# Kernel optimization log

Measured on AMD Instinct MI355X. Metric: run time of the kernel, lower is better.

Reference implementation:

```python
import jax, jax.numpy as jnp
import numpy as np

H, W = 80, 80
LOWPASS = 0.3   # 3DGS low-pass filter added to 2D covariance diagonal
NEAR = 0.2      # near-plane cull depth


def quat_to_rot(q):
    # q: [N,4] (w,x,y,z) -> [N,3,3]
    w, x, y, z = q[..., 0], q[..., 1], q[..., 2], q[..., 3]
    return jnp.stack([
        jnp.stack([1 - 2 * (y * y + z * z), 2 * (x * y - w * z), 2 * (x * z + w * y)], -1),
        jnp.stack([2 * (x * y + w * z), 1 - 2 * (x * x + z * z), 2 * (y * z - w * x)], -1),
        jnp.stack([2 * (x * z - w * y), 2 * (y * z + w * x), 1 - 2 * (x * x + y * y)], -1),
    ], -2)


def setup_inputs() -> dict:
    key = jax.random.key(0)
    k1, k2 = jax.random.split(key)
    vsize = 1.25
    def mids(lo, hi, lim):
        g = np.arange(lo, hi + 1e-6, vsize)
        return ((g[:-1] + g[1:]) / 2.0)[:lim]
    xy = mids(-20.0, 20.0, 200)   # 32 midpoints
    zz = mids(-4.0, 4.0, 16)      # 6 midpoints
    X, Y, Z = np.meshgrid(xy, xy, zz, indexing='ij')
    pc_xyz = jnp.asarray(np.stack([X, Y, Z], -1).reshape(-1, 3), jnp.float32)  # [6144,3]
    N = pc_xyz.shape[0]
    B, NC, C = 1, 6, 32
    vox_features = jax.random.normal(k1, (B, N, C), jnp.float32)
    density = jax.random.normal(k2, (B, N), jnp.float32)
    scales = jnp.full((N, 1), float(np.log(vsize)), jnp.float32)
    rots = jnp.concatenate([jnp.ones((N, 1)), jnp.zeros((N, 3))], -1).astype(jnp.float32)
    # 6 surround cameras at origin, yaw = k*60deg; cam axes: x=right, y=up-ish, z=forward
    yaws = np.arange(NC) * (2 * np.pi / NC)
    f = np.stack([np.cos(yaws), np.sin(yaws), np.zeros(NC)], -1)
    r = np.stack([np.sin(yaws), -np.cos(yaws), np.zeros(NC)], -1)
    u = np.cross(f, r)
    Rw2c = np.stack([r, u, f], 1)  # rows are camera axes -> world2cam rotation [NC,3,3]
    cam_rot = jnp.asarray(Rw2c[None], jnp.float32)          # [B,NC,3,3]
    cam_trans = jnp.zeros((B, NC, 3), jnp.float32)          # [B,NC,3]
    cam_intr = jnp.asarray(np.tile(np.array([45.0, 45.0, W / 2.0, H / 2.0], np.float32), (B, NC, 1)))
    return dict(vox_features=vox_features, density=density, cam_rot=cam_rot,
                cam_trans=cam_trans, cam_intr=cam_intr, pc_xyz=pc_xyz,
                scales=scales, rots=rots)


def _render_one(Rcw, t, intr, pc_xyz, Mcov, opacity, feats):
    # Rcw [3,3], t [3], intr [4]; Mcov [N,3,3] = R*diag(s); opacity [N]; feats [N,C]
    fx, fy, cx, cy = intr[0], intr[1], intr[2], intr[3]
    cam = pc_xyz @ Rcw.T + t                    # [N,3] camera-frame means
    tz = jnp.maximum(cam[:, 2], 1e-6)
    valid = (cam[:, 2] > NEAR).astype(pc_xyz.dtype)
    u = fx * cam[:, 0] / tz + cx
    v = fy * cam[:, 1] / tz + cy
    z0 = jnp.zeros_like(tz)
    J = jnp.stack([jnp.stack([fx / tz, z0, -fx * cam[:, 0] / tz ** 2], -1),
                   jnp.stack([z0, fy / tz, -fy * cam[:, 1] / tz ** 2], -1)], -2)  # [N,2,3]
    A = jnp.einsum('nij,jk->nik', J, Rcw)       # J @ W  [N,2,3]
    Bm = jnp.einsum('nij,njk->nik', A, Mcov)    # [N,2,3]
    cov = jnp.einsum('nij,nkj->nik', Bm, Bm)    # 2D covariance [N,2,2]
    a = cov[:, 0, 0] + LOWPASS
    b = cov[:, 0, 1]
    c = cov[:, 1, 1] + LOWPASS
    det = a * c - b * b
    ia, ib, ic = c / det, -b / det, a / det
    # depth-sort (invalid gaussians pushed to the back)
    order = jnp.argsort(tz + (1.0 - valid) * 1e6)
    u, v, ia, ib, ic = u[order], v[order], ia[order], ib[order], ic[order]
    op_s, feat_s, valid_s = opacity[order], feats[order], valid[order]
    px = jnp.arange(W, dtype=pc_xyz.dtype)
    py = jnp.arange(H, dtype=pc_xyz.dtype)
    dx = px[None, None, :] - u[:, None, None]   # [N,1,W] -> broadcast [N,H,W]
    dy = py[None, :, None] - v[:, None, None]   # [N,H,1]
    power = (-0.5 * (ia[:, None, None] * dx * dx + ic[:, None, None] * dy * dy)
             - ib[:, None, None] * dx * dy)
    g = jnp.exp(jnp.minimum(power, 0.0))
    alpha = jnp.clip(op_s[:, None, None] * g, 0.0, 0.99) * valid_s[:, None, None]
    Tcum = jnp.cumprod(1.0 - alpha, axis=0)
    Texc = jnp.concatenate([jnp.ones((1, H, W), alpha.dtype), Tcum[:-1]], 0)  # exclusive transmittance
    return jnp.einsum('nhw,nc->chw', Texc * alpha, feat_s)


def reference(vox_features, density, cam_rot, cam_trans, cam_intr, pc_xyz, scales, rots):
    Bsz, N, C = vox_features.shape
    Rg = quat_to_rot(rots)                      # [N,3,3]
    s = jnp.exp(scales)                         # [N,1] isotropic scale
    Mcov = Rg * s[:, :, None]                   # R @ diag(s,s,s)
    outs = []
    for b in range(Bsz):
        op = jax.nn.softplus(density[b]).reshape(-1)        # opacity activation
        feats = vox_features[b].reshape(-1, C)
        def rone(args):
            R_, t_, K_ = args
            return _render_one(R_, t_, K_, pc_xyz, Mcov, op, feats)
        out_b = jax.lax.map(rone, (cam_rot[b], cam_trans[b], cam_intr[b]))  # [NC,C,H,W]
        outs.append(out_b)
    return jnp.stack(outs)                      # [B,NC,C,H,W]
```

## Files before the change

### kernel.cpp

```cpp
#include <hip/hip_runtime.h>

#define NEARV    0.2f
#define LOWPASSV 0.3f

constexpr int HH = 80, WW = 80;
constexpr int CFE = 32;
constexpr int NZ = 6;

constexpr int STHREADS = 1024;
constexpr int SWAVES = 16;
constexpr int SBINS = 512;
constexpr int NCELL = 1024;
constexpr int HMAX = NCELL * NZ;

typedef unsigned long long u64;
typedef unsigned int u32;

__global__ __launch_bounds__(1024) void sort_kernel(
    const float* __restrict__ pc_xyz, const float* __restrict__ cam_rot,
    const float* __restrict__ cam_trans, const float* __restrict__ cam_intr,
    const float* __restrict__ density, const float* __restrict__ scales,
    int N, int NC,
    int* __restrict__ counts, float4* __restrict__ hdrA,
    float4* __restrict__ hdrB)
{
  __shared__ u32 skey[NCELL];
  __shared__ u32 spay[NCELL];
  __shared__ u32 whist[SWAVES * SBINS];
  __shared__ u32 binstart[SBINS];
  __shared__ u32 wpart[8];
  __shared__ u32 wsum[SWAVES];
  __shared__ int scount;
  __shared__ int obase;

  const int cam = blockIdx.x;
  const int tid = threadIdx.x;
  const int wv = tid >> 6, ln = tid & 63;
  const float* R = cam_rot + cam*9;
  const float* t = cam_trans + cam*3;
  if (tid == 0) { scount = 0; obase = 0; }
  __syncthreads();

  const int i0 = tid * NZ;
  u32 kk = 0x07FFFFFFu;
  bool valid = false;
  if (i0 < N) {
    float c2 = R[6]*pc_xyz[i0*3+0] + R[7]*pc_xyz[i0*3+1] + R[8]*pc_xyz[i0*3+2] + t[2];
    if (c2 > NEARV) {
      u32 b = __float_as_uint(c2) - 0x3E000000u;
      kk = b < 0x07FFFFFEu ? b : 0x07FFFFFEu;
      valid = true;
    }
  }
  skey[tid] = kk; spay[tid] = (u32)tid;
  u64 vb = __ballot(valid);
  if (ln == 0) atomicAdd(&scount, __popcll(vb));

  for (int pass = 0; pass < 3; ++pass) {
    const int sh = pass * 9;
    for (int i = tid; i < SWAVES*SBINS; i += STHREADS) whist[i] = 0;
    __syncthreads();

    const u32 k = skey[tid];
    const u32 p = spay[tid];
    const int d = (int)((k >> sh) & 511u);
    u64 m = ~0ull;
    #pragma unroll
    for (int b = 0; b < 9; ++b) {
      u64 bb = __ballot((d >> b) & 1);
      m &= ((d >> b) & 1) ? bb : ~bb;
    }
    const u32 lower = (u32)__popcll(m & ((1ull << ln) - 1ull));
    if (lower == 0) whist[(wv << 9) + d] = (u32)__popcll(m);
    __syncthreads();

    if (tid < SBINS) {
      u32 tt[SWAVES];
      #pragma unroll
      for (int w = 0; w < SWAVES; ++w) tt[w] = whist[(w << 9) + tid];
      u32 tot = 0;
      #pragma unroll
      for (int w = 0; w < SWAVES; ++w) { u32 x = tt[w]; whist[(w << 9) + tid] = tot; tot += x; }
      binstart[tid] = tot;
    }
    __syncthreads();
    u32 v = 0, inc = 0;
    if (tid < SBINS) {
      v = binstart[tid]; inc = v;
      #pragma unroll
      for (int off = 1; off < 64; off <<= 1) {
        u32 tq = __shfl_up(inc, off);
        if (ln >= off) inc += tq;
      }
      if (ln == 63) wpart[tid >> 6] = inc;
    }
    __syncthreads();
    if (tid < SBINS) {
      u32 add = 0;
      for (int i = 0; i < (tid >> 6); ++i) add += wpart[i];
      binstart[tid] = add + inc - v;
    }
    __syncthreads();

    const u32 pos = binstart[d] + whist[(wv << 9) + d] + lower;
    skey[pos] = k; spay[pos] = p;
    __syncthreads();
  }

  const int vc = scount;
  const int total = vc * NZ;
  const float* intr = cam_intr + cam*4;
  const float fx = intr[0], fy = intr[1], cx = intr[2], cy = intr[3];
  const float R0=R[0],R1=R[1],R2=R[2],R3=R[3],R4=R[4],R5=R[5],R6=R[6],R7=R[7],R8=R[8];
  const float t0=t[0],t1=t[1],t2=t[2];
  const int b = cam / NC;
  float4* hA = hdrA + (size_t)cam * HMAX;
  float4* hB = hdrB + (size_t)cam * HMAX;

  for (int k0 = 0; k0 < total; k0 += STHREADS) {
    const int kq = k0 + tid;
    bool keep = false;
    float4 va = make_float4(0.f,0.f,0.f,0.f);
    float4 vbh = make_float4(0.f,0.f,0.f,0.f);
    if (kq < total) {
      const int cellp = kq / NZ;
      const int n = (int)spay[cellp] * NZ + (kq - cellp * NZ);
      const float p0 = pc_xyz[n*3+0], p1 = pc_xyz[n*3+1], p2 = pc_xyz[n*3+2];
      const float c0 = R0*p0 + R1*p1 + R2*p2 + t0;
      const float c1 = R3*p0 + R4*p1 + R5*p2 + t1;
      const float c2 = R6*p0 + R7*p1 + R8*p2 + t2;
      const float tz = fmaxf(c2, 1e-6f);
      const float itz = 1.0f / tz;
      const float u = fx*c0*itz + cx;
      const float v = fy*c1*itz + cy;
      const float j00 = fx*itz, j02 = -(fx*c0*itz)*itz;
      const float j11 = fy*itz, j12 = -(fy*c1*itz)*itz;
      const float s = expf(scales[n]);
      const float s2 = s*s;
      const float cov00 = s2*(j00*j00 + j02*j02);
      const float cov01 = s2*(j02*j12);
      const float cov11 = s2*(j11*j11 + j12*j12);
      const float a = cov00 + LOWPASSV, bb = cov01, cc = cov11 + LOWPASSV;
      const float det = a*cc - bb*bb;
      const float idet = 1.0f / det;
      const float mid = 0.5f*(a + cc);
      const float dd = sqrtf(fmaxf(mid*mid - det, 0.f));
      const float r2 = 32.f * (mid + dd);
      const float dens = density[(size_t)b*N + n];
      const float op = fmaxf(dens, 0.f) + log1pf(expf(-fabsf(dens)));
      const float sx = fminf(fmaxf(u, 0.f), (float)(WW-1)) - u;
      const float sy = fminf(fmaxf(v, 0.f), (float)(HH-1)) - v;
      keep = (sx*sx + sy*sy) <= r2;
      va  = make_float4(u, v, cc*idet, -bb*idet);
      vbh = make_float4(a*idet, op, r2, __int_as_float(n));
    }
    const u64 bal = __ballot(keep);
    if (ln == 0) wsum[wv] = (u32)__popcll(bal);
    __syncthreads();
    if (keep) {
      u32 off = 0;
      for (int w = 0; w < wv; ++w) off += wsum[w];
      const int pos = obase + (int)(off + (u32)__popcll(bal & ((1ull << ln) - 1ull)));
      hA[pos] = va; hB[pos] = vbh;
    }
    __syncthreads();
    if (tid == 0) {
      u32 tot = 0;
      #pragma unroll
      for (int w = 0; w < SWAVES; ++w) tot += wsum[w];
      obase += (int)tot;
    }
    __syncthreads();
  }
  if (tid == 0) counts[cam] = obase;
}

__global__ __launch_bounds__(64) void render_kernel(
    const float* __restrict__ vox,
    const float4* __restrict__ hdrA, const float4* __restrict__ hdrB,
    const int* __restrict__ counts,
    float* __restrict__ out, int N, int NC)
{
  __shared__ float4 cA[64], cB[64];
  __shared__ int   cgi[64];
  __shared__ float4 sfeat[64];

  const int cam = blockIdx.y;
  const int tile = blockIdx.x;
  const int tx = tile % (WW/16), ty = tile / (WW/16);
  const int lane = threadIdx.x;
  const int lx = lane & 15, ly = lane >> 4;
  const int px = tx*16 + lx, py = ty*4 + ly;
  const float fpx = (float)px, fpy = (float)py;
  const float tx0 = (float)(tx*16), tx1 = tx0 + 15.f;
  const float ty0 = (float)(ty*4),  ty1 = ty0 + 3.f;
  const int count = counts[cam];
  const int b = cam / NC;
  const float4* hA = hdrA + (size_t)cam * HMAX;
  const float4* hB = hdrB + (size_t)cam * HMAX;
  const float4* voxb = (const float4*)vox + (size_t)b * N * (CFE/4);

  float acc[CFE];
  #pragma unroll
  for (int i = 0; i < CFE; ++i) acc[i] = 0.f;
  float T = 1.0f;
  bool done = false;

  if (count > 0) {
    const int kcf = min(lane, count - 1);
    float4 na = hA[kcf], nb = hB[kcf];

    for (int k0 = 0; k0 < count && !done; k0 += 64) {
      const float4 a0 = na, b0 = nb;
      if (k0 + 64 < count) {
        const int kn = min(k0 + 64 + lane, count - 1);
        na = hA[kn]; nb = hB[kn];
      }
      const int ki = k0 + lane;
      const float ddx = fminf(fmaxf(a0.x, tx0), tx1) - a0.x;
      const float ddy = fminf(fmaxf(a0.y, ty0), ty1) - a0.y;
      const bool hit = (ki < count) && (ddx*ddx + ddy*ddy <= b0.z);
      const u64 m = __ballot(hit);
      const int P = __popcll(m);
      if (P == 0) continue;
      __syncthreads();
      if (hit) {
        const int pos = (int)__popcll(m & ((1ull << lane) - 1ull));
        cA[pos] = a0;
        cB[pos] = b0;
        cgi[pos] = __float_as_int(b0.w);
      }
      __syncthreads();

      const int sl = lane >> 3, sc = lane & 7;
      float4 pf = voxb[(size_t)cgi[min(sl, P - 1)] * (CFE/4) + sc];

      for (int j = 0; j < P; j += 8) {
        sfeat[lane] = pf;
        if (j + 8 < P) {
          const int si = min(j + 8 + sl, P - 1);
          pf = voxb[(size_t)cgi[si] * (CFE/4) + sc];
        }
        __syncthreads();

        float al[8];
        #pragma unroll
        for (int qq = 0; qq < 8; ++qq) {
          const int idx = j + qq;
          const float4 a1 = cA[idx & 63];
          const float4 a2 = cB[idx & 63];
          const float dx = fpx - a1.x, dy = fpy - a1.y;
          const float power = -0.5f*(a1.z*dx*dx + a2.x*dy*dy) - a1.w*dx*dy;
          float av = fminf(a2.y * __expf(fminf(power, 0.f)), 0.99f);
          av = (power > -16.f) ? av : 0.f;
          al[qq] = (idx < P) ? av : 0.f;
        }
        #pragma unroll
        for (int qq = 0; qq < 8; ++qq) {
          const float w = T * al[qq];
          T -= w;
          if (__any(w > 1e-8f)) {
            const float4* fj = &sfeat[qq * 8];
            #pragma unroll
            for (int c8 = 0; c8 < CFE/4; ++c8) {
              const float4 fv = fj[c8];
              acc[c8*4+0] += w*fv.x; acc[c8*4+1] += w*fv.y;
              acc[c8*4+2] += w*fv.z; acc[c8*4+3] += w*fv.w;
            }
          }
        }
        if (__all(T < 1e-4f)) { done = true; break; }
        __syncthreads();
      }
    }
  }
  float* ob = out + (((size_t)cam * CFE) * HH + py) * WW + px;
  #pragma unroll
  for (int c = 0; c < CFE; ++c) ob[(size_t)c * HH * WW] = acc[c];
}

extern "C" void kernel_launch(void* const* d_in, const int* in_sizes, int n_in,
                              void* d_out, int out_size, void* d_ws, size_t ws_size,
                              hipStream_t stream) {
  const float* vox       = (const float*)d_in[0];
  const float* density   = (const float*)d_in[1];
  const float* cam_rot   = (const float*)d_in[2];
  const float* cam_trans = (const float*)d_in[3];
  const float* cam_intr  = (const float*)d_in[4];
  const float* pc_xyz    = (const float*)d_in[5];
  const float* scales    = (const float*)d_in[6];
  float* out = (float*)d_out;

  const int N    = in_sizes[5] / 3;
  const int NCAM = in_sizes[4] / 4;
  const int B    = in_sizes[1] / N;
  const int NC   = NCAM / B;

  unsigned char* ws = (unsigned char*)d_ws;
  int* countsPtr = (int*)ws;
  float4* hdrA = (float4*)(ws + 256);
  float4* hdrB = (float4*)(ws + 256 + (size_t)NCAM * HMAX * sizeof(float4));

  sort_kernel<<<dim3(NCAM), STHREADS, 0, stream>>>(
      pc_xyz, cam_rot, cam_trans, cam_intr, density, scales, N, NC,
      countsPtr, hdrA, hdrB);
  render_kernel<<<dim3((WW/16)*(HH/4), NCAM), 64, 0, stream>>>(
      vox, hdrA, hdrB, countsPtr, out, N, NC);
}
```

Measured before the change: 89.21 us.

## Split render depth list across four waves and compact sort output in one pass

The render kernel now runs four waves per 16x4 tile. Each wave blends one contiguous quarter of the depth-sorted gaussian list into its own partial colour and transmittance. The partial results are then merged back to front through shared memory, which parallelises the serial per-tile compositing loop and removes the block-wide barriers inside it. The sort kernel's compaction is also rewritten to evaluate all six rounds in registers and do a single prefix scan instead of three barriers per round. The trade-offs are that early termination now applies only within each segment, so later segments do work that may be fully occluded, and both kernels use more registers and shared memory.

```diff
diff --git a/kernel.cpp b/kernel.cpp
--- a/kernel.cpp
+++ b/kernel.cpp
@@ -12,6 +12,7 @@
 constexpr int SBINS = 512;
 constexpr int NCELL = 1024;
 constexpr int HMAX = NCELL * NZ;
+constexpr int SEG = 4;
 
 typedef unsigned long long u64;
 typedef unsigned int u32;
@@ -29,16 +30,15 @@
   __shared__ u32 whist[SWAVES * SBINS];
   __shared__ u32 binstart[SBINS];
   __shared__ u32 wpart[8];
-  __shared__ u32 wsum[SWAVES];
+  __shared__ u32 wcnt[6 * SWAVES + 1];
   __shared__ int scount;
-  __shared__ int obase;
 
   const int cam = blockIdx.x;
   const int tid = threadIdx.x;
   const int wv = tid >> 6, ln = tid & 63;
   const float* R = cam_rot + cam*9;
   const float* t = cam_trans + cam*3;
-  if (tid == 0) { scount = 0; obase = 0; }
+  if (tid == 0) scount = 0;
   __syncthreads();
 
   const int i0 = tid * NZ;
@@ -107,8 +107,7 @@
     __syncthreads();
   }
 
-  const int vc = scount;
-  const int total = vc * NZ;
+  const int total = scount * NZ;
   const float* intr = cam_intr + cam*4;
   const float fx = intr[0], fy = intr[1], cx = intr[2], cy = intr[3];
   const float R0=R[0],R1=R[1],R2=R[2],R3=R[3],R4=R[4],R5=R[5],R6=R[6],R7=R[7],R8=R[8];
@@ -117,9 +116,11 @@
   float4* hA = hdrA + (size_t)cam * HMAX;
   float4* hB = hdrB + (size_t)cam * HMAX;
 
-  for (int k0 = 0; k0 < total; k0 += STHREADS) {
-    const int kq = k0 + tid;
-    bool keep = false;
+  float4 rva[6], rvb[6];
+  u32 rkeep = 0;
+  #pragma unroll
+  for (int r = 0; r < 6; ++r) {
+    const int kq = r * STHREADS + tid;
     float4 va = make_float4(0.f,0.f,0.f,0.f);
     float4 vbh = make_float4(0.f,0.f,0.f,0.f);
     if (kq < total) {
@@ -150,45 +151,66 @@
       const float op = fmaxf(dens, 0.f) + log1pf(expf(-fabsf(dens)));
       const float sx = fminf(fmaxf(u, 0.f), (float)(WW-1)) - u;
       const float sy = fminf(fmaxf(v, 0.f), (float)(HH-1)) - v;
-      keep = (sx*sx + sy*sy) <= r2;
+      if (sx*sx + sy*sy <= r2) rkeep |= (1u << r);
       va  = make_float4(u, v, cc*idet, -bb*idet);
       vbh = make_float4(a*idet, op, r2, __int_as_float(n));
     }
-    const u64 bal = __ballot(keep);
-    if (ln == 0) wsum[wv] = (u32)__popcll(bal);
-    __syncthreads();
-    if (keep) {
-      u32 off = 0;
-      for (int w = 0; w < wv; ++w) off += wsum[w];
-      const int pos = obase + (int)(off + (u32)__popcll(bal & ((1ull << ln) - 1ull)));
-      hA[pos] = va; hB[pos] = vbh;
-    }
-    __syncthreads();
-    if (tid == 0) {
-      u32 tot = 0;
+    rva[r] = va; rvb[r] = vbh;
+  }
+
+  u64 bal[6];
+  #pragma unroll
+  for (int r = 0; r < 6; ++r) {
+    bal[r] = __ballot((rkeep >> r) & 1u);
+    if (ln == 0) wcnt[r * SWAVES + wv] = (u32)__popcll(bal[r]);
+  }
+  __syncthreads();
+  {
+    u32 v = 0, inc = 0;
+    if (tid < 96) {
+      v = wcnt[tid]; inc = v;
       #pragma unroll
-      for (int w = 0; w < SWAVES; ++w) tot += wsum[w];
-      obase += (int)tot;
-    }
-    __syncthreads();
-  }
-  if (tid == 0) counts[cam] = obase;
+      for (int off = 1; off < 64; off <<= 1) {
+        u32 tq = __shfl_up(inc, off);
+        if (ln >= off) inc += tq;
+      }
+      if (tid == 63) wpart[0] = inc;
+    }
+    __syncthreads();
+    if (tid < 96) wcnt[tid] = ((tid >= 64) ? wpart[0] : 0u) + inc - v;
+    if (tid == 95) wcnt[96] = wpart[0] + inc;
+    __syncthreads();
+  }
+
+  #pragma unroll
+  for (int r = 0; r < 6; ++r) {
+    if ((rkeep >> r) & 1u) {
+      const int pos = (int)(wcnt[r * SWAVES + wv] +
+                            (u32)__popcll(bal[r] & ((1ull << ln) - 1ull)));
+      hA[pos] = rva[r]; hB[pos] = rvb[r];
+    }
+  }
+  if (tid == 0) counts[cam] = (int)wcnt[96];
 }
 
-__global__ __launch_bounds__(64) void render_kernel(
+__global__ __launch_bounds__(256) void render_kernel(
     const float* __restrict__ vox,
     const float4* __restrict__ hdrA, const float4* __restrict__ hdrB,
     const int* __restrict__ counts,
     float* __restrict__ out, int N, int NC)
 {
-  __shared__ float4 cA[64], cB[64];
-  __shared__ int   cgi[64];
-  __shared__ float4 sfeat[64];
+  __shared__ float4 cA[SEG][64], cB[SEG][64];
+  __shared__ int   cgi[SEG][64];
+  __shared__ float4 sfeat[SEG][64];
+  __shared__ float segC[64][CFE + 1];
+  __shared__ float segP[64];
 
   const int cam = blockIdx.y;
   const int tile = blockIdx.x;
   const int tx = tile % (WW/16), ty = tile / (WW/16);
-  const int lane = threadIdx.x;
+  const int tidb = threadIdx.x;
+  const int wv = tidb >> 6;
+  const int lane = tidb & 63;
   const int lx = lane & 15, ly = lane >> 4;
   const int px = tx*16 + lx, py = ty*4 + ly;
   const float fpx = (float)px, fpy = (float)py;
@@ -200,55 +222,53 @@
   const float4* hB = hdrB + (size_t)cam * HMAX;
   const float4* voxb = (const float4*)vox + (size_t)b * N * (CFE/4);
 
+  const int kb = (count * wv) / SEG;
+  const int ke = (count * (wv + 1)) / SEG;
+
   float acc[CFE];
   #pragma unroll
   for (int i = 0; i < CFE; ++i) acc[i] = 0.f;
   float T = 1.0f;
   bool done = false;
 
-  if (count > 0) {
-    const int kcf = min(lane, count - 1);
+  if (ke > kb) {
+    const int kcf = min(kb + lane, ke - 1);
     float4 na = hA[kcf], nb = hB[kcf];
 
-    for (int k0 = 0; k0 < count && !done; k0 += 64) {
+    for (int k0 = kb; k0 < ke && !done; k0 += 64) {
       const float4 a0 = na, b0 = nb;
-      if (k0 + 64 < count) {
-        const int kn = min(k0 + 64 + lane, count - 1);
+      if (k0 + 64 < ke) {
+        const int kn = min(k0 + 64 + lane, ke - 1);
         na = hA[kn]; nb = hB[kn];
       }
       const int ki = k0 + lane;
       const float ddx = fminf(fmaxf(a0.x, tx0), tx1) - a0.x;
       const float ddy = fminf(fmaxf(a0.y, ty0), ty1) - a0.y;
-      const bool hit = (ki < count) && (ddx*ddx + ddy*ddy <= b0.z);
+      const bool hit = (ki < ke) && (ddx*ddx + ddy*ddy <= b0.z);
       const u64 m = __ballot(hit);
       const int P = __popcll(m);
       if (P == 0) continue;
-      __syncthreads();
       if (hit) {
         const int pos = (int)__popcll(m & ((1ull << lane) - 1ull));
-        cA[pos] = a0;
-        cB[pos] = b0;
-        cgi[pos] = __float_as_int(b0.w);
-      }
-      __syncthreads();
-
+        cA[wv][pos] = a0;
+        cB[wv][pos] = b0;
+        cgi[wv][pos] = __float_as_int(b0.w);
+      }
       const int sl = lane >> 3, sc = lane & 7;
-      float4 pf = voxb[(size_t)cgi[min(sl, P - 1)] * (CFE/4) + sc];
+      float4 pf = voxb[(size_t)cgi[wv][min(sl, P - 1)] * (CFE/4) + sc];
 
       for (int j = 0; j < P; j += 8) {
-        sfeat[lane] = pf;
+        sfeat[wv][lane] = pf;
         if (j + 8 < P) {
           const int si = min(j + 8 + sl, P - 1);
-          pf = voxb[(size_t)cgi[si] * (CFE/4) + sc];
+          pf = voxb[(size_t)cgi[wv][si] * (CFE/4) + sc];
         }
-        __syncthreads();
-
         float al[8];
         #pragma unroll
         for (int qq = 0; qq < 8; ++qq) {
           const int idx = j + qq;
-          const float4 a1 = cA[idx & 63];
-          const float4 a2 = cB[idx & 63];
+          const float4 a1 = cA[wv][idx & 63];
+          const float4 a2 = cB[wv][idx & 63];
           const float dx = fpx - a1.x, dy = fpy - a1.y;
           const float power = -0.5f*(a1.z*dx*dx + a2.x*dy*dy) - a1.w*dx*dy;
           float av = fminf(a2.y * __expf(fminf(power, 0.f)), 0.99f);
@@ -260,7 +280,7 @@
           const float w = T * al[qq];
           T -= w;
           if (__any(w > 1e-8f)) {
-            const float4* fj = &sfeat[qq * 8];
+            const float4* fj = &sfeat[wv][qq * 8];
             #pragma unroll
             for (int c8 = 0; c8 < CFE/4; ++c8) {
               const float4 fv = fj[c8];
@@ -270,13 +290,42 @@
           }
         }
         if (__all(T < 1e-4f)) { done = true; break; }
-        __syncthreads();
-      }
-    }
-  }
-  float* ob = out + (((size_t)cam * CFE) * HH + py) * WW + px;
-  #pragma unroll
-  for (int c = 0; c < CFE; ++c) ob[(size_t)c * HH * WW] = acc[c];
+      }
+    }
+  }
+
+  __syncthreads();
+  if (wv == 3) {
+    #pragma unroll
+    for (int c = 0; c < CFE; ++c) segC[lane][c] = acc[c];
+    segP[lane] = T;
+  }
+  __syncthreads();
+  if (wv == 2) {
+    #pragma unroll
+    for (int c = 0; c < CFE; ++c) acc[c] += T * segC[lane][c];
+    T *= segP[lane];
+    #pragma unroll
+    for (int c = 0; c < CFE; ++c) segC[lane][c] = acc[c];
+    segP[lane] = T;
+  }
+  __syncthreads();
+  if (wv == 1) {
+    #pragma unroll
+    for (int c = 0; c < CFE; ++c) acc[c] += T * segC[lane][c];
+    T *= segP[lane];
+    #pragma unroll
+    for (int c = 0; c < CFE; ++c) segC[lane][c] = acc[c];
+    segP[lane] = T;
+  }
+  __syncthreads();
+  if (wv == 0) {
+    #pragma unroll
+    for (int c = 0; c < CFE; ++c) acc[c] += T * segC[lane][c];
+    float* ob = out + (((size_t)cam * CFE) * HH + py) * WW + px;
+    #pragma unroll
+    for (int c = 0; c < CFE; ++c) ob[(size_t)c * HH * WW] = acc[c];
+  }
 }
 
 extern "C" void kernel_launch(void* const* d_in, const int* in_sizes, int n_in,
@@ -304,6 +353,6 @@
   sort_kernel<<<dim3(NCAM), STHREADS, 0, stream>>>(
       pc_xyz, cam_rot, cam_trans, cam_intr, density, scales, N, NC,
       countsPtr, hdrA, hdrB);
-  render_kernel<<<dim3((WW/16)*(HH/4), NCAM), 64, 0, stream>>>(
+  render_kernel<<<dim3((WW/16)*(HH/4), NCAM), 256, 0, stream>>>(
       vox, hdrA, hdrB, countsPtr, out, N, NC);
 }
```

Result: slower. 232.9 us (+161.1%).

## Split per-gaussian projection out of sort kernel into parallel proj kernel

Applied to the files above, without the earlier changes.

The sort kernel now only radix-sorts cells by depth and writes the cell order and count. A new proj_kernel spreads projection and covariance computation across many blocks per camera instead of one 1024-thread block looping. Culled gaussians are no longer compacted; they are kept in place with r2 set to -1. This adds a kernel launch, and the render kernel must now iterate over the uncompacted list and rely on the r2 sentinel to skip culled entries.

```diff
diff --git a/kernel.cpp b/kernel.cpp
--- a/kernel.cpp
+++ b/kernel.cpp
@@ -18,34 +18,30 @@
 
 __global__ __launch_bounds__(1024) void sort_kernel(
     const float* __restrict__ pc_xyz, const float* __restrict__ cam_rot,
-    const float* __restrict__ cam_trans, const float* __restrict__ cam_intr,
-    const float* __restrict__ density, const float* __restrict__ scales,
-    int N, int NC,
-    int* __restrict__ counts, float4* __restrict__ hdrA,
-    float4* __restrict__ hdrB)
+    const float* __restrict__ cam_trans, int N,
+    int* __restrict__ counts, int* __restrict__ cellord)
 {
   __shared__ u32 skey[NCELL];
   __shared__ u32 spay[NCELL];
   __shared__ u32 whist[SWAVES * SBINS];
   __shared__ u32 binstart[SBINS];
   __shared__ u32 wpart[8];
-  __shared__ u32 wsum[SWAVES];
   __shared__ int scount;
-  __shared__ int obase;
 
   const int cam = blockIdx.x;
   const int tid = threadIdx.x;
   const int wv = tid >> 6, ln = tid & 63;
   const float* R = cam_rot + cam*9;
-  const float* t = cam_trans + cam*3;
-  if (tid == 0) { scount = 0; obase = 0; }
+  const float R20 = R[6], R21 = R[7], R22 = R[8];
+  const float t2  = cam_trans[cam*3+2];
+  if (tid == 0) scount = 0;
   __syncthreads();
 
   const int i0 = tid * NZ;
   u32 kk = 0x07FFFFFFu;
   bool valid = false;
   if (i0 < N) {
-    float c2 = R[6]*pc_xyz[i0*3+0] + R[7]*pc_xyz[i0*3+1] + R[8]*pc_xyz[i0*3+2] + t[2];
+    float c2 = R20*pc_xyz[i0*3+0] + R21*pc_xyz[i0*3+1] + R22*pc_xyz[i0*3+2] + t2;
     if (c2 > NEARV) {
       u32 b = __float_as_uint(c2) - 0x3E000000u;
       kk = b < 0x07FFFFFEu ? b : 0x07FFFFFEu;
@@ -75,12 +71,12 @@
     __syncthreads();
 
     if (tid < SBINS) {
-      u32 tt[SWAVES];
+      u32 t[SWAVES];
       #pragma unroll
-      for (int w = 0; w < SWAVES; ++w) tt[w] = whist[(w << 9) + tid];
+      for (int w = 0; w < SWAVES; ++w) t[w] = whist[(w << 9) + tid];
       u32 tot = 0;
       #pragma unroll
-      for (int w = 0; w < SWAVES; ++w) { u32 x = tt[w]; whist[(w << 9) + tid] = tot; tot += x; }
+      for (int w = 0; w < SWAVES; ++w) { u32 x = t[w]; whist[(w << 9) + tid] = tot; tot += x; }
       binstart[tid] = tot;
     }
     __syncthreads();
@@ -89,8 +85,8 @@
       v = binstart[tid]; inc = v;
       #pragma unroll
       for (int off = 1; off < 64; off <<= 1) {
-        u32 tq = __shfl_up(inc, off);
-        if (ln >= off) inc += tq;
+        u32 t = __shfl_up(inc, off);
+        if (ln >= off) inc += t;
       }
       if (ln == 63) wpart[tid >> 6] = inc;
     }
@@ -108,71 +104,60 @@
   }
 
   const int vc = scount;
-  const int total = vc * NZ;
+  if (tid < vc) cellord[(size_t)cam * NCELL + tid] = (int)spay[tid];
+  if (tid == 0) counts[cam] = vc * NZ;
+}
+
+__global__ __launch_bounds__(256) void proj_kernel(
+    const float* __restrict__ pc_xyz, const float* __restrict__ cam_rot,
+    const float* __restrict__ cam_trans, const float* __restrict__ cam_intr,
+    const float* __restrict__ density, const float* __restrict__ scales,
+    int N, int NC,
+    const int* __restrict__ counts, const int* __restrict__ cellord,
+    float4* __restrict__ hdrA, float4* __restrict__ hdrB)
+{
+  const int cam = blockIdx.y;
+  const int kq = blockIdx.x * 256 + threadIdx.x;
+  if (kq >= counts[cam]) return;
+
+  const int cellp = kq / NZ;
+  const int n = cellord[(size_t)cam * NCELL + cellp] * NZ + (kq - cellp * NZ);
+
+  const float* R = cam_rot + cam*9;
+  const float* t = cam_trans + cam*3;
   const float* intr = cam_intr + cam*4;
   const float fx = intr[0], fy = intr[1], cx = intr[2], cy = intr[3];
-  const float R0=R[0],R1=R[1],R2=R[2],R3=R[3],R4=R[4],R5=R[5],R6=R[6],R7=R[7],R8=R[8];
-  const float t0=t[0],t1=t[1],t2=t[2];
   const int b = cam / NC;
-  float4* hA = hdrA + (size_t)cam * HMAX;
-  float4* hB = hdrB + (size_t)cam * HMAX;
-
-  for (int k0 = 0; k0 < total; k0 += STHREADS) {
-    const int kq = k0 + tid;
-    bool keep = false;
-    float4 va = make_float4(0.f,0.f,0.f,0.f);
-    float4 vbh = make_float4(0.f,0.f,0.f,0.f);
-    if (kq < total) {
-      const int cellp = kq / NZ;
-      const int n = (int)spay[cellp] * NZ + (kq - cellp * NZ);
-      const float p0 = pc_xyz[n*3+0], p1 = pc_xyz[n*3+1], p2 = pc_xyz[n*3+2];
-      const float c0 = R0*p0 + R1*p1 + R2*p2 + t0;
-      const float c1 = R3*p0 + R4*p1 + R5*p2 + t1;
-      const float c2 = R6*p0 + R7*p1 + R8*p2 + t2;
-      const float tz = fmaxf(c2, 1e-6f);
-      const float itz = 1.0f / tz;
-      const float u = fx*c0*itz + cx;
-      const float v = fy*c1*itz + cy;
-      const float j00 = fx*itz, j02 = -(fx*c0*itz)*itz;
-      const float j11 = fy*itz, j12 = -(fy*c1*itz)*itz;
-      const float s = expf(scales[n]);
-      const float s2 = s*s;
-      const float cov00 = s2*(j00*j00 + j02*j02);
-      const float cov01 = s2*(j02*j12);
-      const float cov11 = s2*(j11*j11 + j12*j12);
-      const float a = cov00 + LOWPASSV, bb = cov01, cc = cov11 + LOWPASSV;
-      const float det = a*cc - bb*bb;
-      const float idet = 1.0f / det;
-      const float mid = 0.5f*(a + cc);
-      const float dd = sqrtf(fmaxf(mid*mid - det, 0.f));
-      const float r2 = 32.f * (mid + dd);
-      const float dens = density[(size_t)b*N + n];
-      const float op = fmaxf(dens, 0.f) + log1pf(expf(-fabsf(dens)));
-      const float sx = fminf(fmaxf(u, 0.f), (float)(WW-1)) - u;
-      const float sy = fminf(fmaxf(v, 0.f), (float)(HH-1)) - v;
-      keep = (sx*sx + sy*sy) <= r2;
-      va  = make_float4(u, v, cc*idet, -bb*idet);
-      vbh = make_float4(a*idet, op, r2, __int_as_float(n));
-    }
-    const u64 bal = __ballot(keep);
-    if (ln == 0) wsum[wv] = (u32)__popcll(bal);
-    __syncthreads();
-    if (keep) {
-      u32 off = 0;
-      for (int w = 0; w < wv; ++w) off += wsum[w];
-      const int pos = obase + (int)(off + (u32)__popcll(bal & ((1ull << ln) - 1ull)));
-      hA[pos] = va; hB[pos] = vbh;
-    }
-    __syncthreads();
-    if (tid == 0) {
-      u32 tot = 0;
-      #pragma unroll
-      for (int w = 0; w < SWAVES; ++w) tot += wsum[w];
-      obase += (int)tot;
-    }
-    __syncthreads();
-  }
-  if (tid == 0) counts[cam] = obase;
+
+  const float p0 = pc_xyz[n*3+0], p1 = pc_xyz[n*3+1], p2 = pc_xyz[n*3+2];
+  const float c0 = R[0]*p0 + R[1]*p1 + R[2]*p2 + t[0];
+  const float c1 = R[3]*p0 + R[4]*p1 + R[5]*p2 + t[1];
+  const float c2 = R[6]*p0 + R[7]*p1 + R[8]*p2 + t[2];
+  const float tz = fmaxf(c2, 1e-6f);
+  const float itz = 1.0f / tz;
+  const float u = fx*c0*itz + cx;
+  const float v = fy*c1*itz + cy;
+  const float j00 = fx*itz, j02 = -(fx*c0*itz)*itz;
+  const float j11 = fy*itz, j12 = -(fy*c1*itz)*itz;
+  const float s = expf(scales[n]);
+  const float s2 = s*s;
+  const float cov00 = s2*(j00*j00 + j02*j02);
+  const float cov01 = s2*(j02*j12);
+  const float cov11 = s2*(j11*j11 + j12*j12);
+  const float a = cov00 + LOWPASSV, bb = cov01, cc = cov11 + LOWPASSV;
+  const float det = a*cc - bb*bb;
+  const float idet = 1.0f / det;
+  const float mid = 0.5f*(a + cc);
+  const float dd = sqrtf(fmaxf(mid*mid - det, 0.f));
+  float r2 = 32.f * (mid + dd);
+  const float dens = density[(size_t)b*N + n];
+  const float op = fmaxf(dens, 0.f) + log1pf(expf(-fabsf(dens)));
+  const float sx = fminf(fmaxf(u, 0.f), (float)(WW-1)) - u;
+  const float sy = fminf(fmaxf(v, 0.f), (float)(HH-1)) - v;
+  if (sx*sx + sy*sy > r2) r2 = -1.0f;
+
+  hdrA[(size_t)cam * HMAX + kq] = make_float4(u, v, cc*idet, -bb*idet);
+  hdrB[(size_t)cam * HMAX + kq] = make_float4(a*idet, op, r2, __int_as_float(n));
 }
 
 __global__ __launch_bounds__(64) void render_kernel(
@@ -298,12 +283,15 @@
 
   unsigned char* ws = (unsigned char*)d_ws;
   int* countsPtr = (int*)ws;
-  float4* hdrA = (float4*)(ws + 256);
-  float4* hdrB = (float4*)(ws + 256 + (size_t)NCAM * HMAX * sizeof(float4));
+  int* cellord   = (int*)(ws + 256);
+  float4* hdrA   = (float4*)(ws + 32768);
+  float4* hdrB   = (float4*)(ws + 32768 + (size_t)NCAM * HMAX * sizeof(float4));
 
   sort_kernel<<<dim3(NCAM), STHREADS, 0, stream>>>(
+      pc_xyz, cam_rot, cam_trans, N, countsPtr, cellord);
+  proj_kernel<<<dim3((HMAX + 255) / 256, NCAM), 256, 0, stream>>>(
       pc_xyz, cam_rot, cam_trans, cam_intr, density, scales, N, NC,
-      countsPtr, hdrA, hdrB);
+      countsPtr, cellord, hdrA, hdrB);
   render_kernel<<<dim3((WW/16)*(HH/4), NCAM), 64, 0, stream>>>(
       vox, hdrA, hdrB, countsPtr, out, N, NC);
 }
```

Result: faster. 83.86 us (-6.0%).
